# Performance work log

Hardware: AMD Instinct MI355X
Metric: run time of the kernel (lower is better)

## Reference

```python
import jax, jax.numpy as jnp
import numpy as np

N_NODES = 100000


def gcn_conv(x, edge_index, edge_weight, W, b):
    """PyG GCNConv: add self-loops (weight 1), symmetric deg^-1/2 norm,
    linear transform, scatter-add aggregation over destination nodes, + bias."""
    n = x.shape[0]
    src = jnp.concatenate([edge_index[0], jnp.arange(n, dtype=edge_index.dtype)])
    dst = jnp.concatenate([edge_index[1], jnp.arange(n, dtype=edge_index.dtype)])
    ew = jnp.concatenate([edge_weight, jnp.ones((n,), dtype=x.dtype)])
    # weighted degree over destinations (symmetric graph assumed as in GCN norm)
    deg = jax.ops.segment_sum(ew, dst, num_segments=n)
    dinv = jnp.where(deg > 0, jax.lax.rsqrt(deg), 0.0).astype(x.dtype)
    norm = dinv[src] * ew * dinv[dst]                    # [E+N]
    h = x @ W                                            # [N, out]
    msg = h[src] * norm[:, None]                         # gather + scale
    agg = jax.ops.segment_sum(msg, dst, num_segments=n)  # scatter-add
    return agg + b


def setup_inputs() -> dict:
    key = jax.random.key(0)
    k = jax.random.split(key, 8)
    d_in, d_hid, d_out = 128, 64, 2
    n_edges = 3200000
    x = jax.random.normal(k[0], (N_NODES, d_in), dtype=jnp.float32)
    edge_index = jax.random.randint(k[1], (2, n_edges), 0, N_NODES, dtype=jnp.int64)
    edge_weight = jax.random.uniform(k[2], (n_edges,), dtype=jnp.float32)
    # Glorot-ish init for linear weights, zeros for bias (PyG default)
    W1 = jax.random.normal(k[3], (d_in, d_hid), dtype=jnp.float32) / np.sqrt(d_in)
    b1 = jnp.zeros((d_hid,), dtype=jnp.float32)
    W2 = jax.random.normal(k[4], (d_hid, d_out), dtype=jnp.float32) / np.sqrt(d_hid)
    b2 = jnp.zeros((d_out,), dtype=jnp.float32)
    return {"x": x, "edge_index": edge_index, "edge_weight": edge_weight,
            "W1": W1, "b1": b1, "W2": W2, "b2": b2}


def reference(x, edge_index, edge_weight, W1, b1, W2, b2):
    h = gcn_conv(x, edge_index, edge_weight, W1, b1)
    h = jax.nn.relu(h)
    out = gcn_conv(h, edge_index, edge_weight, W2, b2)
    return out
```

## Files before the change

kernel.cpp:

```cpp
#include <hip/hip_runtime.h>
#include <hip/hip_bf16.h>
#include <hip/hip_fp16.h>


#define DIN  128
#define DHID 64
#define BSH  7
#define BCAP 5000
#define SCHUNK 12544
#define BMAX 800

typedef _Float16 half8 __attribute__((ext_vector_type(8)));
typedef float    f32x4 __attribute__((ext_vector_type(4)));

__global__ __launch_bounds__(1024) void k_hist(const int* __restrict__ ei,
                                               int* __restrict__ histT,
                                               int E, int chunk, int B, int C) {
    __shared__ int h[4][BMAX + 1];
    for (int t = threadIdx.x; t < 4 * (BMAX + 1); t += 1024)
        ((int*)h)[t] = 0;
    __syncthreads();
    int c = blockIdx.x;
    int rep = (threadIdx.x >> 6) & 3;
    int e0 = c * chunk, e1 = min(E, e0 + chunk);
    for (int e = e0 + threadIdx.x; e < e1; e += 1024)
        atomicAdd(&h[rep][ei[E + e] >> BSH], 1);
    __syncthreads();
    for (int t = threadIdx.x; t < B; t += 1024)
        histT[(size_t)t * C + c] = h[0][t] + h[1][t] + h[2][t] + h[3][t];
}

__global__ __launch_bounds__(256) void k_scan1(int* __restrict__ histT,
                                               int* __restrict__ tot, int C) {
    __shared__ int sm[256];
    int b = blockIdx.x, t = threadIdx.x;
    size_t base = (size_t)b * C;
    int v = histT[base + t];
    sm[t] = v;
    __syncthreads();
    for (int off = 1; off < 256; off <<= 1) {
        int add = (t >= off) ? sm[t - off] : 0;
        __syncthreads();
        sm[t] += add;
        __syncthreads();
    }
    histT[base + t] = sm[t] - v;
    if (t == 255) tot[b] = sm[t];
}

__global__ __launch_bounds__(1024) void k_scan2(const int* __restrict__ tot,
                                                int* __restrict__ bb, int B) {
    __shared__ int sm[1024];
    int t = threadIdx.x;
    int v = (t < B) ? tot[t] : 0;
    sm[t] = v;
    __syncthreads();
    for (int off = 1; off < 1024; off <<= 1) {
        int add = (t >= off) ? sm[t - off] : 0;
        __syncthreads();
        sm[t] += add;
        __syncthreads();
    }
    if (t < B) {
        bb[t] = sm[t] - v;
        if (t == B - 1) bb[B] = sm[t];
    }
}

__global__ __launch_bounds__(1024) void k_scatter(const int* __restrict__ ei,
                                                  const float* __restrict__ ew,
                                                  const int* __restrict__ histT,
                                                  const int* __restrict__ bb,
                                                  int2* __restrict__ ebuf,
                                                  int E, int chunk, int B, int C) {
    __shared__ int eidx[SCHUNK];
    __shared__ int lbase[BMAX];
    __shared__ int lcur[BMAX];
    __shared__ int gbase[BMAX];
    int c = blockIdx.x, t = threadIdx.x;
    int e0 = c * chunk, e1 = min(E, e0 + chunk), m = e1 - e0;

    for (int b = t; b < B; b += 1024) lcur[b] = 0;
    __syncthreads();
    for (int q = t; q < m; q += 1024)
        atomicAdd(&lcur[ei[E + e0 + q] >> BSH], 1);
    __syncthreads();
    int v = (t < B) ? lcur[t] : 0;
    eidx[t] = v;
    __syncthreads();
    for (int off = 1; off < 1024; off <<= 1) {
        int add = (t >= off) ? eidx[t - off] : 0;
        __syncthreads();
        eidx[t] += add;
        __syncthreads();
    }
    if (t < B) {
        lbase[t] = eidx[t] - v;
        gbase[t] = histT[(size_t)t * C + c] + bb[t];
        lcur[t] = 0;
    }
    __syncthreads();
    for (int q = t; q < m; q += 1024) {
        int b = ei[E + e0 + q] >> BSH;
        int pos = lbase[b] + atomicAdd(&lcur[b], 1);
        eidx[pos] = q;
    }
    __syncthreads();
    for (int q = t; q < m; q += 1024) {
        int e = e0 + eidx[q];
        int s = ei[e];
        int d = ei[E + e];
        float w = ew[e];
        int b = d >> BSH;
        int gpos = gbase[b] + (q - lbase[b]);
        ebuf[gpos] = make_int2(s | ((d & 127) << 24), __float_as_int(w));
    }
}

__global__ __launch_bounds__(512) void k_build(const int2* __restrict__ ebuf,
                                               const int* __restrict__ bb,
                                               int* __restrict__ rp,
                                               float* __restrict__ dinv,
                                               int2* __restrict__ csw,
                                               int N, int E) {
    __shared__ int2  stage[BCAP];
    __shared__ int   cnt4[4][132];
    __shared__ float dsum4[4][132];
    __shared__ int   lrp[128];
    __shared__ int   cur[128];
    __shared__ int   sm[512];
    int b = blockIdx.x, t = threadIdx.x;
    if (t < 128) {
#pragma unroll
        for (int r = 0; r < 4; ++r) { cnt4[r][t] = 0; dsum4[r][t] = 0.0f; }
        cur[t] = 0;
    }
    __syncthreads();
    int p0 = bb[b], p1 = bb[b + 1];
    int m = p1 - p0;
    bool fits = (m <= BCAP);
    int rep = (t >> 6) & 3;
    for (int p = p0 + t; p < p1; p += 512) {
        int2 v = ebuf[p];
        if (fits) stage[p - p0] = v;
        int ln = (((unsigned)v.x) >> 24) & 127;
        atomicAdd(&cnt4[rep][ln], 1);
        atomicAdd(&dsum4[rep][ln], __int_as_float(v.y));
    }
    __syncthreads();
    int cv = 0;
    if (t < 128) cv = cnt4[0][t] + cnt4[1][t] + cnt4[2][t] + cnt4[3][t];
    sm[t] = cv;
    __syncthreads();
    for (int off = 1; off < 128; off <<= 1) {
        int add = (t >= off) ? sm[t - off] : 0;
        __syncthreads();
        sm[t] += add;
        __syncthreads();
    }
    if (t < 128) {
        lrp[t] = sm[t] - cv + p0;
        int d = (b << BSH) + t;
        if (d < N) {
            rp[d]   = lrp[t];
            float ds = dsum4[0][t] + dsum4[1][t] + dsum4[2][t] + dsum4[3][t];
            dinv[d] = rsqrtf(1.0f + ds);
        }
    }
    if (b == 0 && t == 0) rp[N] = E;
    __syncthreads();
    for (int q = t; q < m; q += 512) {
        int2 v = fits ? stage[q] : ebuf[p0 + q];
        int ln = (((unsigned)v.x) >> 24) & 127;
        int r = atomicAdd(&cur[ln], 1);
        csw[lrp[ln] + r] = make_int2(v.x & 0xFFFFFF, v.y);
    }
}

__global__ __launch_bounds__(256) void k_gemm1(const float* __restrict__ x,
                                               const float* __restrict__ W1,
                                               __half* __restrict__ h1, int N) {
    __shared__ _Float16 As[64][136];
    __shared__ _Float16 Bs[64][136];
    int t = threadIdx.x;
    int wave = t >> 6, lane = t & 63;
    int r0 = blockIdx.x * 64;

    for (int idx = t; idx < DIN * DHID; idx += 256) {
        int k = idx >> 6, c = idx & 63;
        Bs[c][k] = (_Float16)W1[idx];
    }
    const float4* xv = (const float4*)x;
    for (int idx = t; idx < 64 * 32; idx += 256) {
        int r = idx >> 5, c4 = idx & 31;
        int rr = r0 + r;
        float4 v = (rr < N) ? xv[(size_t)rr * 32 + c4]
                            : make_float4(0.f, 0.f, 0.f, 0.f);
        As[r][c4 * 4 + 0] = (_Float16)v.x;
        As[r][c4 * 4 + 1] = (_Float16)v.y;
        As[r][c4 * 4 + 2] = (_Float16)v.z;
        As[r][c4 * 4 + 3] = (_Float16)v.w;
    }
    __syncthreads();

    int row = lane & 15;
    int kg  = lane >> 4;
    f32x4 acc0 = {0.f,0.f,0.f,0.f}, acc1 = {0.f,0.f,0.f,0.f};
    f32x4 acc2 = {0.f,0.f,0.f,0.f}, acc3 = {0.f,0.f,0.f,0.f};
#pragma unroll
    for (int kc = 0; kc < 4; ++kc) {
        half8 a = *(const half8*)&As[wave * 16 + row][kc * 32 + kg * 8];
        half8 b0 = *(const half8*)&Bs[ 0 + row][kc * 32 + kg * 8];
        half8 b1 = *(const half8*)&Bs[16 + row][kc * 32 + kg * 8];
        half8 b2 = *(const half8*)&Bs[32 + row][kc * 32 + kg * 8];
        half8 b3 = *(const half8*)&Bs[48 + row][kc * 32 + kg * 8];
        acc0 = __builtin_amdgcn_mfma_f32_16x16x32_f16(a, b0, acc0, 0, 0, 0);
        acc1 = __builtin_amdgcn_mfma_f32_16x16x32_f16(a, b1, acc1, 0, 0, 0);
        acc2 = __builtin_amdgcn_mfma_f32_16x16x32_f16(a, b2, acc2, 0, 0, 0);
        acc3 = __builtin_amdgcn_mfma_f32_16x16x32_f16(a, b3, acc3, 0, 0, 0);
    }
#pragma unroll
    for (int reg = 0; reg < 4; ++reg) {
        int rr = r0 + wave * 16 + kg * 4 + reg;
        if (rr < N) {
            int col = lane & 15;
            size_t base = (size_t)rr * DHID;
            h1[base + col +  0] = __float2half(acc0[reg]);
            h1[base + col + 16] = __float2half(acc1[reg]);
            h1[base + col + 32] = __float2half(acc2[reg]);
            h1[base + col + 48] = __float2half(acc3[reg]);
        }
    }
}

__global__ __launch_bounds__(256) void k_agg1(const __half* __restrict__ h1h,
                                              const int* __restrict__ rp,
                                              const int2* __restrict__ csw,
                                              const float* __restrict__ dinv,
                                              const float* __restrict__ b1,
                                              const float* __restrict__ W2,
                                              float* __restrict__ h2, int N) {
    int lane = threadIdx.x & 63;
    int i = (blockIdx.x * 256 + threadIdx.x) >> 6;
    if (i >= N) return;
    float bias = b1[lane];
    float w2a = W2[lane * 2];
    float w2b = W2[lane * 2 + 1];
    int s0 = __builtin_amdgcn_readfirstlane(rp[i]);
    int e0 = __builtin_amdgcn_readfirstlane(rp[i + 1]);
    float acc = 0.0f;
    int p = s0;
    for (; p + 8 <= e0; p += 8) {
        int2 eA = csw[p],     eB = csw[p + 1], eC = csw[p + 2], eD = csw[p + 3];
        int2 eE = csw[p + 4], eF = csw[p + 5], eG = csw[p + 6], eH = csw[p + 7];
        int sA = __builtin_amdgcn_readfirstlane(eA.x);
        int sB = __builtin_amdgcn_readfirstlane(eB.x);
        int sC = __builtin_amdgcn_readfirstlane(eC.x);
        int sD = __builtin_amdgcn_readfirstlane(eD.x);
        int sE = __builtin_amdgcn_readfirstlane(eE.x);
        int sF = __builtin_amdgcn_readfirstlane(eF.x);
        int sG = __builtin_amdgcn_readfirstlane(eG.x);
        int sH = __builtin_amdgcn_readfirstlane(eH.x);
        float wA = __uint_as_float(__builtin_amdgcn_readfirstlane(eA.y)) * dinv[sA];
        float wB = __uint_as_float(__builtin_amdgcn_readfirstlane(eB.y)) * dinv[sB];
        float wC = __uint_as_float(__builtin_amdgcn_readfirstlane(eC.y)) * dinv[sC];
        float wD = __uint_as_float(__builtin_amdgcn_readfirstlane(eD.y)) * dinv[sD];
        float wE = __uint_as_float(__builtin_amdgcn_readfirstlane(eE.y)) * dinv[sE];
        float wF = __uint_as_float(__builtin_amdgcn_readfirstlane(eF.y)) * dinv[sF];
        float wG = __uint_as_float(__builtin_amdgcn_readfirstlane(eG.y)) * dinv[sG];
        float wH = __uint_as_float(__builtin_amdgcn_readfirstlane(eH.y)) * dinv[sH];
        float hA = __half2float(h1h[(size_t)sA * DHID + lane]);
        float hB = __half2float(h1h[(size_t)sB * DHID + lane]);
        float hC = __half2float(h1h[(size_t)sC * DHID + lane]);
        float hD = __half2float(h1h[(size_t)sD * DHID + lane]);
        float hE = __half2float(h1h[(size_t)sE * DHID + lane]);
        float hF = __half2float(h1h[(size_t)sF * DHID + lane]);
        float hG = __half2float(h1h[(size_t)sG * DHID + lane]);
        float hH = __half2float(h1h[(size_t)sH * DHID + lane]);
        acc = fmaf(wA, hA, acc);
        acc = fmaf(wB, hB, acc);
        acc = fmaf(wC, hC, acc);
        acc = fmaf(wD, hD, acc);
        acc = fmaf(wE, hE, acc);
        acc = fmaf(wF, hF, acc);
        acc = fmaf(wG, hG, acc);
        acc = fmaf(wH, hH, acc);
    }
    for (; p + 4 <= e0; p += 4) {
        int2 eA = csw[p], eB = csw[p + 1], eC = csw[p + 2], eD = csw[p + 3];
        int sA = __builtin_amdgcn_readfirstlane(eA.x);
        int sB = __builtin_amdgcn_readfirstlane(eB.x);
        int sC = __builtin_amdgcn_readfirstlane(eC.x);
        int sD = __builtin_amdgcn_readfirstlane(eD.x);
        float wA = __uint_as_float(__builtin_amdgcn_readfirstlane(eA.y)) * dinv[sA];
        float wB = __uint_as_float(__builtin_amdgcn_readfirstlane(eB.y)) * dinv[sB];
        float wC = __uint_as_float(__builtin_amdgcn_readfirstlane(eC.y)) * dinv[sC];
        float wD = __uint_as_float(__builtin_amdgcn_readfirstlane(eD.y)) * dinv[sD];
        float hA = __half2float(h1h[(size_t)sA * DHID + lane]);
        float hB = __half2float(h1h[(size_t)sB * DHID + lane]);
        float hC = __half2float(h1h[(size_t)sC * DHID + lane]);
        float hD = __half2float(h1h[(size_t)sD * DHID + lane]);
        acc = fmaf(wA, hA, acc);
        acc = fmaf(wB, hB, acc);
        acc = fmaf(wC, hC, acc);
        acc = fmaf(wD, hD, acc);
    }
    for (; p < e0; ++p) {
        int2 eA = csw[p];
        int sA = __builtin_amdgcn_readfirstlane(eA.x);
        float wA = __uint_as_float(__builtin_amdgcn_readfirstlane(eA.y)) * dinv[sA];
        acc = fmaf(wA, __half2float(h1h[(size_t)sA * DHID + lane]), acc);
    }
    float di = dinv[i];
    acc = (acc + di * __half2float(h1h[(size_t)i * DHID + lane])) * di;
    acc = fmaxf(acc + bias, 0.0f);
    float o0 = acc * w2a, o1 = acc * w2b;
    for (int off = 32; off > 0; off >>= 1) {
        o0 += __shfl_xor(o0, off);
        o1 += __shfl_xor(o1, off);
    }
    if (lane == 0) {
        h2[i * 2]     = o0;
        h2[i * 2 + 1] = o1;
    }
}

__global__ __launch_bounds__(256) void k_prop2(const float* __restrict__ h2,
                                               const int* __restrict__ rp,
                                               const int2* __restrict__ csw,
                                               const float* __restrict__ dinv,
                                               const float* __restrict__ b2,
                                               float* __restrict__ out, int N) {
    const float2* h2v = (const float2*)h2;
    int lane = threadIdx.x & 63;
    int i = (blockIdx.x * 256 + threadIdx.x) >> 6;
    if (i >= N) return;
    int s0 = rp[i], e0 = rp[i + 1];
    float a0 = 0.0f, a1 = 0.0f;
    for (int p = s0 + lane; p < e0; p += 64) {
        int2 ed = csw[p];
        float w = __int_as_float(ed.y) * dinv[ed.x];
        float2 hv = h2v[ed.x];
        a0 = fmaf(w, hv.x, a0);
        a1 = fmaf(w, hv.y, a1);
    }
    for (int off = 32; off > 0; off >>= 1) {
        a0 += __shfl_xor(a0, off);
        a1 += __shfl_xor(a1, off);
    }
    if (lane == 0) {
        float di = dinv[i];
        out[i * 2]     = di * (a0 + di * h2[i * 2])     + b2[0];
        out[i * 2 + 1] = di * (a1 + di * h2[i * 2 + 1]) + b2[1];
    }
}

extern "C" void kernel_launch(void* const* d_in, const int* in_sizes, int n_in,
                              void* d_out, int out_size, void* d_ws, size_t ws_size,
                              hipStream_t stream) {
    const float* x  = (const float*)d_in[0];
    const int*   ei = (const int*)d_in[1];
    const float* ew = (const float*)d_in[2];
    const float* W1 = (const float*)d_in[3];
    const float* b1 = (const float*)d_in[4];
    const float* W2 = (const float*)d_in[5];
    const float* b2 = (const float*)d_in[6];
    float* out = (float*)d_out;

    const int N = in_sizes[0] / DIN;
    const int E = in_sizes[2];

    const int C = 256;
    const int B = (N + 127) >> BSH;
    const int chunk = (E + C - 1) / C;

    char* w0 = (char*)d_ws;
    float* dinv  = (float*)w0;
    int*   rp    = (int*)(dinv + N);
    int*   histT = rp + (N + 4);
    int*   tot   = histT + (size_t)B * C;
    int*   bb    = tot + B;
    size_t off_csw = ((size_t)((char*)(bb + B + 1) - w0) + 15) & ~(size_t)15;
    int2*  csw  = (int2*)(w0 + off_csw);
    int2*  ebuf = csw + E;
    __half* h1  = (__half*)ebuf;
    float* h2   = (float*)(h1 + (size_t)N * DHID);

    k_hist<<<C, 1024, 0, stream>>>(ei, histT, E, chunk, B, C);
    k_scan1<<<B, 256, 0, stream>>>(histT, tot, C);
    k_scan2<<<1, 1024, 0, stream>>>(tot, bb, B);
    k_scatter<<<C, 1024, 0, stream>>>(ei, ew, histT, bb, ebuf, E, chunk, B, C);
    k_build<<<B, 512, 0, stream>>>(ebuf, bb, rp, dinv, csw, N, E);

    const int GB = (N + 63) / 64;
    k_gemm1<<<GB, 256, 0, stream>>>(x, W1, h1, N);

    const int GW = ((size_t)N * 64 + 255) / 256;
    k_agg1<<<GW, 256, 0, stream>>>(h1, rp, csw, dinv, b1, W2, h2, N);
    k_prop2<<<GW, 256, 0, stream>>>(h2, rp, csw, dinv, b2, out, N);
}
```

Baseline: 380.0 us.

## Sub-bucket CSR edges by source range and aggregate in source-range phases

The CSR build now splits each destination's edge list into four sub-segments by source-index range (s>>15), recording four row pointers per node. The aggregation kernel gives each wave 13 destination nodes and sweeps the four source ranges in order, accumulating partial sums in shared memory. This keeps the h1 gather working set per phase to about a quarter of the table, aiming for better L2/cache locality across concurrently running waves. It costs extra row-pointer storage, more loop overhead, per-phase block barriers, and fewer waves in flight, which may limit latency hiding.

```diff
diff --git a/kernel.cpp b/kernel.cpp
--- a/kernel.cpp
+++ b/kernel.cpp
@@ -9,6 +9,7 @@
 #define BCAP 5000
 #define SCHUNK 12544
 #define BMAX 800
+#define NPW  13
 
 typedef _Float16 half8 __attribute__((ext_vector_type(8)));
 typedef float    f32x4 __attribute__((ext_vector_type(4)));
@@ -119,22 +120,22 @@
 
 __global__ __launch_bounds__(512) void k_build(const int2* __restrict__ ebuf,
                                                const int* __restrict__ bb,
-                                               int* __restrict__ rp,
+                                               int* __restrict__ rpx,
                                                float* __restrict__ dinv,
                                                int2* __restrict__ csw,
                                                int N, int E) {
     __shared__ int2  stage[BCAP];
-    __shared__ int   cnt4[4][132];
+    __shared__ int   cnt[128][4];
     __shared__ float dsum4[4][132];
-    __shared__ int   lrp[128];
-    __shared__ int   cur[128];
+    __shared__ int   base2[128][4];
+    __shared__ int   cur2[128][4];
     __shared__ int   sm[512];
     int b = blockIdx.x, t = threadIdx.x;
     if (t < 128) {
 #pragma unroll
-        for (int r = 0; r < 4; ++r) { cnt4[r][t] = 0; dsum4[r][t] = 0.0f; }
-        cur[t] = 0;
-    }
+        for (int k = 0; k < 4; ++k) { cnt[t][k] = 0; cur2[t][k] = 0; }
+    }
+    dsum4[t >> 7][t & 127] = 0.0f;
     __syncthreads();
     int p0 = bb[b], p1 = bb[b + 1];
     int m = p1 - p0;
@@ -144,12 +145,13 @@
         int2 v = ebuf[p];
         if (fits) stage[p - p0] = v;
         int ln = (((unsigned)v.x) >> 24) & 127;
-        atomicAdd(&cnt4[rep][ln], 1);
+        int k  = (v.x & 0xFFFFFF) >> 15;
+        atomicAdd(&cnt[ln][k], 1);
         atomicAdd(&dsum4[rep][ln], __int_as_float(v.y));
     }
     __syncthreads();
     int cv = 0;
-    if (t < 128) cv = cnt4[0][t] + cnt4[1][t] + cnt4[2][t] + cnt4[3][t];
+    if (t < 128) cv = cnt[t][0] + cnt[t][1] + cnt[t][2] + cnt[t][3];
     sm[t] = cv;
     __syncthreads();
     for (int off = 1; off < 128; off <<= 1) {
@@ -159,21 +161,29 @@
         __syncthreads();
     }
     if (t < 128) {
-        lrp[t] = sm[t] - cv + p0;
+        int lrp = sm[t] - cv + p0;
         int d = (b << BSH) + t;
+        int acc2 = lrp;
+#pragma unroll
+        for (int k = 0; k < 4; ++k) {
+            base2[t][k] = acc2;
+            if (d < N) rpx[d * 4 + k] = acc2;
+            acc2 += cnt[t][k];
+        }
         if (d < N) {
-            rp[d]   = lrp[t];
             float ds = dsum4[0][t] + dsum4[1][t] + dsum4[2][t] + dsum4[3][t];
             dinv[d] = rsqrtf(1.0f + ds);
         }
     }
-    if (b == 0 && t == 0) rp[N] = E;
+    if (b == 0 && t == 0) rpx[4 * N] = E;
     __syncthreads();
     for (int q = t; q < m; q += 512) {
         int2 v = fits ? stage[q] : ebuf[p0 + q];
         int ln = (((unsigned)v.x) >> 24) & 127;
-        int r = atomicAdd(&cur[ln], 1);
-        csw[lrp[ln] + r] = make_int2(v.x & 0xFFFFFF, v.y);
+        int s  = v.x & 0xFFFFFF;
+        int k  = s >> 15;
+        int r = atomicAdd(&cur2[ln][k], 1);
+        csw[base2[ln][k] + r] = make_int2(s, v.y);
     }
 }
 
@@ -233,100 +243,112 @@
     }
 }
 
-__global__ __launch_bounds__(256) void k_agg1(const __half* __restrict__ h1h,
-                                              const int* __restrict__ rp,
-                                              const int2* __restrict__ csw,
-                                              const float* __restrict__ dinv,
-                                              const float* __restrict__ b1,
-                                              const float* __restrict__ W2,
-                                              float* __restrict__ h2, int N) {
-    int lane = threadIdx.x & 63;
-    int i = (blockIdx.x * 256 + threadIdx.x) >> 6;
-    if (i >= N) return;
+__global__ __launch_bounds__(256, 8) void k_aggW(const __half* __restrict__ h1h,
+                                                 const int* __restrict__ rpx,
+                                                 const int2* __restrict__ csw,
+                                                 const float* __restrict__ dinv,
+                                                 const float* __restrict__ b1,
+                                                 const float* __restrict__ W2,
+                                                 float* __restrict__ h2, int N) {
+    __shared__ float accs[4][NPW][64];
+    int t = threadIdx.x, lane = t & 63, wl = t >> 6;
+    int i0 = (blockIdx.x * 4 + wl) * NPW;
+    for (int j = 0; j < NPW; ++j) accs[wl][j][lane] = 0.0f;
+    for (int k = 0; k < 4; ++k) {
+        for (int j = 0; j < NPW; ++j) {
+            int i = i0 + j;
+            if (i >= N) break;
+            int p  = __builtin_amdgcn_readfirstlane(rpx[i * 4 + k]);
+            int pe = __builtin_amdgcn_readfirstlane(rpx[i * 4 + k + 1]);
+            float acc = 0.0f;
+            for (; p + 8 <= pe; p += 8) {
+                int2 eA = csw[p],     eB = csw[p + 1], eC = csw[p + 2], eD = csw[p + 3];
+                int2 eE = csw[p + 4], eF = csw[p + 5], eG = csw[p + 6], eH = csw[p + 7];
+                int sA = __builtin_amdgcn_readfirstlane(eA.x);
+                int sB = __builtin_amdgcn_readfirstlane(eB.x);
+                int sC = __builtin_amdgcn_readfirstlane(eC.x);
+                int sD = __builtin_amdgcn_readfirstlane(eD.x);
+                int sE = __builtin_amdgcn_readfirstlane(eE.x);
+                int sF = __builtin_amdgcn_readfirstlane(eF.x);
+                int sG = __builtin_amdgcn_readfirstlane(eG.x);
+                int sH = __builtin_amdgcn_readfirstlane(eH.x);
+                float wA = __uint_as_float(__builtin_amdgcn_readfirstlane(eA.y)) * dinv[sA];
+                float wB = __uint_as_float(__builtin_amdgcn_readfirstlane(eB.y)) * dinv[sB];
+                float wC = __uint_as_float(__builtin_amdgcn_readfirstlane(eC.y)) * dinv[sC];
+                float wD = __uint_as_float(__builtin_amdgcn_readfirstlane(eD.y)) * dinv[sD];
+                float wE = __uint_as_float(__builtin_amdgcn_readfirstlane(eE.y)) * dinv[sE];
+                float wF = __uint_as_float(__builtin_amdgcn_readfirstlane(eF.y)) * dinv[sF];
+                float wG = __uint_as_float(__builtin_amdgcn_readfirstlane(eG.y)) * dinv[sG];
+                float wH = __uint_as_float(__builtin_amdgcn_readfirstlane(eH.y)) * dinv[sH];
+                float hA = __half2float(h1h[(size_t)sA * DHID + lane]);
+                float hB = __half2float(h1h[(size_t)sB * DHID + lane]);
+                float hC = __half2float(h1h[(size_t)sC * DHID + lane]);
+                float hD = __half2float(h1h[(size_t)sD * DHID + lane]);
+                float hE = __half2float(h1h[(size_t)sE * DHID + lane]);
+                float hF = __half2float(h1h[(size_t)sF * DHID + lane]);
+                float hG = __half2float(h1h[(size_t)sG * DHID + lane]);
+                float hH = __half2float(h1h[(size_t)sH * DHID + lane]);
+                acc = fmaf(wA, hA, acc);
+                acc = fmaf(wB, hB, acc);
+                acc = fmaf(wC, hC, acc);
+                acc = fmaf(wD, hD, acc);
+                acc = fmaf(wE, hE, acc);
+                acc = fmaf(wF, hF, acc);
+                acc = fmaf(wG, hG, acc);
+                acc = fmaf(wH, hH, acc);
+            }
+            for (; p + 4 <= pe; p += 4) {
+                int2 eA = csw[p], eB = csw[p + 1], eC = csw[p + 2], eD = csw[p + 3];
+                int sA = __builtin_amdgcn_readfirstlane(eA.x);
+                int sB = __builtin_amdgcn_readfirstlane(eB.x);
+                int sC = __builtin_amdgcn_readfirstlane(eC.x);
+                int sD = __builtin_amdgcn_readfirstlane(eD.x);
+                float wA = __uint_as_float(__builtin_amdgcn_readfirstlane(eA.y)) * dinv[sA];
+                float wB = __uint_as_float(__builtin_amdgcn_readfirstlane(eB.y)) * dinv[sB];
+                float wC = __uint_as_float(__builtin_amdgcn_readfirstlane(eC.y)) * dinv[sC];
+                float wD = __uint_as_float(__builtin_amdgcn_readfirstlane(eD.y)) * dinv[sD];
+                float hA = __half2float(h1h[(size_t)sA * DHID + lane]);
+                float hB = __half2float(h1h[(size_t)sB * DHID + lane]);
+                float hC = __half2float(h1h[(size_t)sC * DHID + lane]);
+                float hD = __half2float(h1h[(size_t)sD * DHID + lane]);
+                acc = fmaf(wA, hA, acc);
+                acc = fmaf(wB, hB, acc);
+                acc = fmaf(wC, hC, acc);
+                acc = fmaf(wD, hD, acc);
+            }
+            for (; p < pe; ++p) {
+                int2 eA = csw[p];
+                int sA = __builtin_amdgcn_readfirstlane(eA.x);
+                float wA = __uint_as_float(__builtin_amdgcn_readfirstlane(eA.y)) * dinv[sA];
+                acc = fmaf(wA, __half2float(h1h[(size_t)sA * DHID + lane]), acc);
+            }
+            accs[wl][j][lane] += acc;
+        }
+        __syncthreads();
+    }
     float bias = b1[lane];
-    float w2a = W2[lane * 2];
-    float w2b = W2[lane * 2 + 1];
-    int s0 = __builtin_amdgcn_readfirstlane(rp[i]);
-    int e0 = __builtin_amdgcn_readfirstlane(rp[i + 1]);
-    float acc = 0.0f;
-    int p = s0;
-    for (; p + 8 <= e0; p += 8) {
-        int2 eA = csw[p],     eB = csw[p + 1], eC = csw[p + 2], eD = csw[p + 3];
-        int2 eE = csw[p + 4], eF = csw[p + 5], eG = csw[p + 6], eH = csw[p + 7];
-        int sA = __builtin_amdgcn_readfirstlane(eA.x);
-        int sB = __builtin_amdgcn_readfirstlane(eB.x);
-        int sC = __builtin_amdgcn_readfirstlane(eC.x);
-        int sD = __builtin_amdgcn_readfirstlane(eD.x);
-        int sE = __builtin_amdgcn_readfirstlane(eE.x);
-        int sF = __builtin_amdgcn_readfirstlane(eF.x);
-        int sG = __builtin_amdgcn_readfirstlane(eG.x);
-        int sH = __builtin_amdgcn_readfirstlane(eH.x);
-        float wA = __uint_as_float(__builtin_amdgcn_readfirstlane(eA.y)) * dinv[sA];
-        float wB = __uint_as_float(__builtin_amdgcn_readfirstlane(eB.y)) * dinv[sB];
-        float wC = __uint_as_float(__builtin_amdgcn_readfirstlane(eC.y)) * dinv[sC];
-        float wD = __uint_as_float(__builtin_amdgcn_readfirstlane(eD.y)) * dinv[sD];
-        float wE = __uint_as_float(__builtin_amdgcn_readfirstlane(eE.y)) * dinv[sE];
-        float wF = __uint_as_float(__builtin_amdgcn_readfirstlane(eF.y)) * dinv[sF];
-        float wG = __uint_as_float(__builtin_amdgcn_readfirstlane(eG.y)) * dinv[sG];
-        float wH = __uint_as_float(__builtin_amdgcn_readfirstlane(eH.y)) * dinv[sH];
-        float hA = __half2float(h1h[(size_t)sA * DHID + lane]);
-        float hB = __half2float(h1h[(size_t)sB * DHID + lane]);
-        float hC = __half2float(h1h[(size_t)sC * DHID + lane]);
-        float hD = __half2float(h1h[(size_t)sD * DHID + lane]);
-        float hE = __half2float(h1h[(size_t)sE * DHID + lane]);
-        float hF = __half2float(h1h[(size_t)sF * DHID + lane]);
-        float hG = __half2float(h1h[(size_t)sG * DHID + lane]);
-        float hH = __half2float(h1h[(size_t)sH * DHID + lane]);
-        acc = fmaf(wA, hA, acc);
-        acc = fmaf(wB, hB, acc);
-        acc = fmaf(wC, hC, acc);
-        acc = fmaf(wD, hD, acc);
-        acc = fmaf(wE, hE, acc);
-        acc = fmaf(wF, hF, acc);
-        acc = fmaf(wG, hG, acc);
-        acc = fmaf(wH, hH, acc);
-    }
-    for (; p + 4 <= e0; p += 4) {
-        int2 eA = csw[p], eB = csw[p + 1], eC = csw[p + 2], eD = csw[p + 3];
-        int sA = __builtin_amdgcn_readfirstlane(eA.x);
-        int sB = __builtin_amdgcn_readfirstlane(eB.x);
-        int sC = __builtin_amdgcn_readfirstlane(eC.x);
-        int sD = __builtin_amdgcn_readfirstlane(eD.x);
-        float wA = __uint_as_float(__builtin_amdgcn_readfirstlane(eA.y)) * dinv[sA];
-        float wB = __uint_as_float(__builtin_amdgcn_readfirstlane(eB.y)) * dinv[sB];
-        float wC = __uint_as_float(__builtin_amdgcn_readfirstlane(eC.y)) * dinv[sC];
-        float wD = __uint_as_float(__builtin_amdgcn_readfirstlane(eD.y)) * dinv[sD];
-        float hA = __half2float(h1h[(size_t)sA * DHID + lane]);
-        float hB = __half2float(h1h[(size_t)sB * DHID + lane]);
-        float hC = __half2float(h1h[(size_t)sC * DHID + lane]);
-        float hD = __half2float(h1h[(size_t)sD * DHID + lane]);
-        acc = fmaf(wA, hA, acc);
-        acc = fmaf(wB, hB, acc);
-        acc = fmaf(wC, hC, acc);
-        acc = fmaf(wD, hD, acc);
-    }
-    for (; p < e0; ++p) {
-        int2 eA = csw[p];
-        int sA = __builtin_amdgcn_readfirstlane(eA.x);
-        float wA = __uint_as_float(__builtin_amdgcn_readfirstlane(eA.y)) * dinv[sA];
-        acc = fmaf(wA, __half2float(h1h[(size_t)sA * DHID + lane]), acc);
-    }
-    float di = dinv[i];
-    acc = (acc + di * __half2float(h1h[(size_t)i * DHID + lane])) * di;
-    acc = fmaxf(acc + bias, 0.0f);
-    float o0 = acc * w2a, o1 = acc * w2b;
-    for (int off = 32; off > 0; off >>= 1) {
-        o0 += __shfl_xor(o0, off);
-        o1 += __shfl_xor(o1, off);
-    }
-    if (lane == 0) {
-        h2[i * 2]     = o0;
-        h2[i * 2 + 1] = o1;
+    float w2a = W2[lane * 2], w2b = W2[lane * 2 + 1];
+    for (int j = 0; j < NPW; ++j) {
+        int i = i0 + j;
+        if (i >= N) break;
+        float di = dinv[i];
+        float self = __half2float(h1h[(size_t)i * DHID + lane]);
+        float a = (accs[wl][j][lane] + di * self) * di;
+        a = fmaxf(a + bias, 0.0f);
+        float o0 = a * w2a, o1 = a * w2b;
+        for (int off = 32; off > 0; off >>= 1) {
+            o0 += __shfl_xor(o0, off);
+            o1 += __shfl_xor(o1, off);
+        }
+        if (lane == 0) {
+            h2[i * 2]     = o0;
+            h2[i * 2 + 1] = o1;
+        }
     }
 }
 
 __global__ __launch_bounds__(256) void k_prop2(const float* __restrict__ h2,
-                                               const int* __restrict__ rp,
+                                               const int* __restrict__ rpx,
                                                const int2* __restrict__ csw,
                                                const float* __restrict__ dinv,
                                                const float* __restrict__ b2,
@@ -335,7 +357,7 @@
     int lane = threadIdx.x & 63;
     int i = (blockIdx.x * 256 + threadIdx.x) >> 6;
     if (i >= N) return;
-    int s0 = rp[i], e0 = rp[i + 1];
+    int s0 = rpx[i * 4], e0 = rpx[i * 4 + 4];
     float a0 = 0.0f, a1 = 0.0f;
     for (int p = s0 + lane; p < e0; p += 64) {
         int2 ed = csw[p];
@@ -376,8 +398,8 @@
 
     char* w0 = (char*)d_ws;
     float* dinv  = (float*)w0;
-    int*   rp    = (int*)(dinv + N);
-    int*   histT = rp + (N + 4);
+    int*   rpx   = (int*)(dinv + N);
+    int*   histT = rpx + (4 * N + 8);
     int*   tot   = histT + (size_t)B * C;
     int*   bb    = tot + B;
     size_t off_csw = ((size_t)((char*)(bb + B + 1) - w0) + 15) & ~(size_t)15;
@@ -390,12 +412,15 @@
     k_scan1<<<B, 256, 0, stream>>>(histT, tot, C);
     k_scan2<<<1, 1024, 0, stream>>>(tot, bb, B);
     k_scatter<<<C, 1024, 0, stream>>>(ei, ew, histT, bb, ebuf, E, chunk, B, C);
-    k_build<<<B, 512, 0, stream>>>(ebuf, bb, rp, dinv, csw, N, E);
+    k_build<<<B, 512, 0, stream>>>(ebuf, bb, rpx, dinv, csw, N, E);
 
     const int GB = (N + 63) / 64;
     k_gemm1<<<GB, 256, 0, stream>>>(x, W1, h1, N);
 
+    const int WAVES = (N + NPW - 1) / NPW;
+    const int GAW = (WAVES + 3) / 4;
+    k_aggW<<<GAW, 256, 0, stream>>>(h1, rpx, csw, dinv, b1, W2, h2, N);
+
     const int GW = ((size_t)N * 64 + 255) / 256;
-    k_agg1<<<GW, 256, 0, stream>>>(h1, rp, csw, dinv, b1, W2, h2, N);
-    k_prop2<<<GW, 256, 0, stream>>>(h2, rp, csw, dinv, b2, out, N);
-}
+    k_prop2<<<GW, 256, 0, stream>>>(h2, rpx, csw, dinv, b2, out, N);
+}
```

Measured after the change: 410.0 us. 1.08x slower.
